# Kernel tuning notes

Measured on AMD Instinct MI355X. Metric: run time of the kernel, lower is better.

## Reference

```python
import jax, jax.numpy as jnp
import numpy as np

D_MODEL = 1024
NUM_HEADS = 16
HEAD_DIM = D_MODEL // NUM_HEADS


def setup_inputs() -> dict:
    key = jax.random.key(0)
    ks = jax.random.split(key, 10)
    B, SQ, SK = 2, 2048, 2048
    scale = 1.0 / np.sqrt(D_MODEL)
    inp = {
        "x1": jax.random.normal(ks[0], (B, SQ, D_MODEL), jnp.float32),
        "x2": jax.random.normal(ks[1], (B, SK, D_MODEL), jnp.float32),
        "Wq": jax.random.normal(ks[2], (D_MODEL, D_MODEL), jnp.float32) * scale,
        "bq": jnp.zeros((D_MODEL,), jnp.float32),
        "Wk": jax.random.normal(ks[3], (D_MODEL, D_MODEL), jnp.float32) * scale,
        "bk": jnp.zeros((D_MODEL,), jnp.float32),
        "Wv": jax.random.normal(ks[4], (D_MODEL, D_MODEL), jnp.float32) * scale,
        "bv": jnp.zeros((D_MODEL,), jnp.float32),
        "Wo": jax.random.normal(ks[5], (D_MODEL, D_MODEL), jnp.float32) * scale,
        "bo": jnp.zeros((D_MODEL,), jnp.float32),
    }
    return inp


def reference(x1, x2, Wq, bq, Wk, bk, Wv, bv, Wo, bo):
    B, SQ, _ = x1.shape
    SK = x2.shape[1]
    # projections, then split into heads: [B, H, S, Dh]
    def split_heads(t, S):
        return t.reshape(B, S, NUM_HEADS, HEAD_DIM).transpose(0, 2, 1, 3)
    Q = split_heads(x1 @ Wq + bq, SQ)
    K = split_heads(x2 @ Wk + bk, SK)
    V = split_heads(x2 @ Wv + bv, SK)
    # note: original scales by 1/head_dim**0.5
    scores = jnp.einsum("bhqd,bhkd->bhqk", Q, K) / jnp.sqrt(
        jnp.asarray(HEAD_DIM, Q.dtype))
    attn = jax.nn.softmax(scores, axis=-1)
    ctx = jnp.einsum("bhqk,bhkd->bhqd", attn, V)
    ctx = ctx.transpose(0, 2, 1, 3).reshape(B, SQ, D_MODEL)
    return ctx @ Wo + bo
```

## Files before the change

kernel.cpp:

```cpp
#include <hip/hip_runtime.h>
#include <stdint.h>


typedef unsigned short u16b;
typedef __attribute__((ext_vector_type(4))) short short4v;
typedef __attribute__((ext_vector_type(8))) short short8v;
typedef __attribute__((ext_vector_type(4))) float float4v;
typedef __attribute__((ext_vector_type(2))) unsigned int uint2v;

#if __has_builtin(__builtin_amdgcn_exp2f)
__device__ __forceinline__ float exp2_fast(float x){ return __builtin_amdgcn_exp2f(x); }
#else
__device__ __forceinline__ float exp2_fast(float x){ return exp2f(x); }
#endif

__device__ __forceinline__ float bf2f(u16b u) {
  union { unsigned int i; float f; } v; v.i = ((unsigned int)u) << 16; return v.f;
}
__device__ __forceinline__ u16b f2bf(float f) {
  union { float f; unsigned int i; } v; v.f = f;
  return (u16b)((v.i + 0x7fffu + ((v.i >> 16) & 1u)) >> 16);
}
__device__ __forceinline__ void gl_lds16(const u16b* g, u16b* l) {
  __builtin_amdgcn_global_load_lds(
      (const __attribute__((address_space(1))) void*)g,
      (__attribute__((address_space(3))) void*)l, 16, 0, 0);
}

__global__ __launch_bounds__(256) void cvt2_bf16(
    const float* __restrict__ s0, const float* __restrict__ s1,
    u16b* __restrict__ d0, u16b* __restrict__ d1, int n4) {
  const float* src = blockIdx.y ? s1 : s0;
  u16b* dst = blockIdx.y ? d1 : d0;
  int i = blockIdx.x * blockDim.x + threadIdx.x;
  int stride = gridDim.x * blockDim.x;
  for (; i < n4; i += stride) {
    float4v v = ((const float4v*)src)[i];
    short4v o;
    o[0]=(short)f2bf(v[0]); o[1]=(short)f2bf(v[1]);
    o[2]=(short)f2bf(v[2]); o[3]=(short)f2bf(v[3]);
    ((short4v*)dst)[i] = o;
  }
}

__global__ __launch_bounds__(256) void transposeW(
    const float* __restrict__ W0, const float* __restrict__ W1,
    const float* __restrict__ W2, const float* __restrict__ W3,
    u16b* __restrict__ out) {
  __shared__ u16b tile[32][33];
  const int z = blockIdx.z;
  const float* src = (z==0) ? W0 : (z==1) ? W1 : (z==2) ? W2 : W3;
  u16b* dst = out + (size_t)z * (1024*1024);
  const int x = threadIdx.x, y = threadIdx.y;
  const int bx = blockIdx.x * 32, by = blockIdx.y * 32;
#pragma unroll
  for (int j=0;j<4;++j)
    tile[y*4+j][x] = f2bf(src[(size_t)(by + y*4+j)*1024 + bx + x]);
  __syncthreads();
#pragma unroll
  for (int j=0;j<4;++j)
    dst[(size_t)(bx + y*4+j)*1024 + by + x] = tile[x][y*4+j];
}

template<int BN, bool OUT_F32>
__device__ __forceinline__ void gemm_core(
    const u16b* __restrict__ A, const u16b* __restrict__ Bt,
    const float* __restrict__ bias, void* __restrict__ Cv,
    int N, int K, int bm, int bn) {
  constexpr int NT = BN / 32;
  __shared__ __align__(16) u16b As[128*32];
  __shared__ __align__(16) u16b Bs[BN*32];
  const int tid = threadIdx.x;
  const int lane = tid & 63, wave = tid >> 6;
  const int wm = wave >> 1, wn = wave & 1;
  const int l15 = lane & 15, l4 = lane >> 4;
  float4v acc[4][NT];
#pragma unroll
  for (int i=0;i<4;++i)
#pragma unroll
    for (int j=0;j<NT;++j) acc[i][j] = (float4v){0.f,0.f,0.f,0.f};

  const int swz = (l15 >> 1) & 3;

  for (int k0 = 0; k0 < K; k0 += 32) {
    __syncthreads();
    {
      int row = tid >> 2, seg = tid & 3;
      int segg0 = seg ^ ((row >> 1) & 3);
      int row2 = row + 64;
      int segg1 = seg ^ ((row2 >> 1) & 3);
      gl_lds16(&A[(size_t)(bm+row )*K + k0 + segg0*8], &As[tid*8]);
      gl_lds16(&A[(size_t)(bm+row2)*K + k0 + segg1*8], &As[(tid+256)*8]);
      gl_lds16(&Bt[(size_t)(bn+row )*K + k0 + segg0*8], &Bs[tid*8]);
      if (BN == 128)
        gl_lds16(&Bt[(size_t)(bn+row2)*K + k0 + segg1*8], &Bs[(tid+256)*8]);
    }
    __syncthreads();
    short8v af[4], bf[NT];
#pragma unroll
    for (int mt=0;mt<4;++mt)
      af[mt] = *(const short8v*)&As[(wm*64+mt*16+l15)*32 + ((l4 ^ swz)*8)];
#pragma unroll
    for (int nt=0;nt<NT;++nt)
      bf[nt] = *(const short8v*)&Bs[(wn*(BN/2)+nt*16+l15)*32 + ((l4 ^ swz)*8)];
#pragma unroll
    for (int mt=0;mt<4;++mt)
#pragma unroll
      for (int nt=0;nt<NT;++nt)
        acc[mt][nt] = __builtin_amdgcn_mfma_f32_16x16x32_bf16(af[mt], bf[nt], acc[mt][nt], 0, 0, 0);
  }

#pragma unroll
  for (int nt=0;nt<NT;++nt) {
    int col = bn + wn*(BN/2) + nt*16 + l15;
    float bb = bias[col];
#pragma unroll
    for (int mt=0;mt<4;++mt) {
      int row0 = bm + wm*64 + mt*16 + l4*4;
#pragma unroll
      for (int r=0;r<4;++r) {
        float v = acc[mt][nt][r] + bb;
        if (OUT_F32) ((float*)Cv)[(size_t)(row0+r)*N + col] = v;
        else         ((u16b*)Cv)[(size_t)(row0+r)*N + col] = f2bf(v);
      }
    }
  }
}

__global__ __launch_bounds__(256) void gemm_qkv(
    const u16b* __restrict__ x1b, const u16b* __restrict__ x2b,
    const u16b* __restrict__ WT, const float* __restrict__ bq,
    const float* __restrict__ bk, const float* __restrict__ bv,
    u16b* __restrict__ out) {
  const int z = blockIdx.z;
  const u16b* A = (z == 0) ? x1b : x2b;
  const u16b* Bt = WT + (size_t)z * (1024*1024);
  const float* bias = (z == 0) ? bq : (z == 1) ? bk : bv;
  u16b* C = out + (size_t)z * (4u*1024*1024);
  gemm_core<128,false>(A, Bt, bias, C, 1024, 1024, blockIdx.y*128, blockIdx.x*128);
}

__global__ __launch_bounds__(256) void gemm_out(
    const u16b* __restrict__ A, const u16b* __restrict__ Bt,
    const float* __restrict__ bias, float* __restrict__ C) {
  gemm_core<64,true>(A, Bt, bias, C, 1024, 1024, blockIdx.y*128, blockIdx.x*64);
}

__global__ __launch_bounds__(256) void attn128(
    const u16b* __restrict__ Q, const u16b* __restrict__ Kg,
    const u16b* __restrict__ Vg, u16b* __restrict__ O) {
  __shared__ __align__(16) u16b Ks[64*64];
  __shared__ __align__(16) u16b Vs[64*72];
  __shared__ __align__(16) u16b Ps[4*2*16*72];
  const int tid = threadIdx.x;
  const int lane = tid & 63, wave = tid >> 6;
  const int l15 = lane & 15, l4 = lane >> 4;
  const int h = blockIdx.y, b = blockIdx.z;
  const int q0 = blockIdx.x * 128;
  const size_t seqbase = (size_t)b * 2048;
  const int colh = h * 64;
  u16b* Pw = Ps + wave * 2304;

  const float qscale = 0.125f * 1.4426950408889634f;
  short8v qf[2][2];
#pragma unroll
  for (int g=0; g<2; ++g) {
    size_t qrow = seqbase + q0 + wave*32 + g*16 + l15;
#pragma unroll
    for (int ks=0; ks<2; ++ks) {
      short8v raw = *(const short8v*)&Q[qrow*1024 + colh + ks*32 + l4*8];
      short8v s;
#pragma unroll
      for (int i=0;i<8;++i) s[i] = (short)f2bf(bf2f((u16b)raw[i]) * qscale);
      qf[g][ks] = s;
    }
  }

  float lpart[2] = {0.f, 0.f};
  float4v oacc[2][4];
#pragma unroll
  for (int g=0; g<2; ++g)
#pragma unroll
    for (int nb=0; nb<4; ++nb) oacc[g][nb] = (float4v){0.f,0.f,0.f,0.f};

  const int vseg = tid >> 5;
  const int vrp  = tid & 31;

  for (int kt = 0; kt < 32; ++kt) {
    const size_t kvbase = seqbase + (size_t)kt*64;
    __syncthreads();
#pragma unroll
    for (int j=0; j<2; ++j) {
      int idx = j*256 + tid;
      int row = idx >> 3, seg = idx & 7;
      int segg = seg ^ (row & 7);
      gl_lds16(&Kg[(kvbase+row)*1024 + colh + segg*8], &Ks[idx*8]);
    }
    {
      short8v v0 = *(const short8v*)&Vg[(kvbase + 2*vrp    )*1024 + colh + vseg*8];
      short8v v1 = *(const short8v*)&Vg[(kvbase + 2*vrp + 1)*1024 + colh + vseg*8];
#pragma unroll
      for (int i=0;i<8;++i) {
        unsigned int val = (unsigned int)(u16b)v0[i] | ((unsigned int)(u16b)v1[i] << 16);
        *(unsigned int*)&Vs[(vseg*8+i)*72 + 2*vrp] = val;
      }
    }
    __syncthreads();

    float4v sacc[2][4];
#pragma unroll
    for (int g=0; g<2; ++g)
#pragma unroll
      for (int nb=0; nb<4; ++nb) sacc[g][nb] = (float4v){0.f,0.f,0.f,0.f};
#pragma unroll
    for (int nb=0; nb<4; ++nb)
#pragma unroll
      for (int ks=0; ks<2; ++ks) {
        short8v kf = *(const short8v*)&Ks[(nb*16+l15)*64 + (((ks*4+l4) ^ (l15 & 7))*8)];
        sacc[0][nb] = __builtin_amdgcn_mfma_f32_16x16x32_bf16(kf, qf[0][ks], sacc[0][nb], 0, 0, 0);
        sacc[1][nb] = __builtin_amdgcn_mfma_f32_16x16x32_bf16(kf, qf[1][ks], sacc[1][nb], 0, 0, 0);
      }

#pragma unroll
    for (int g=0; g<2; ++g) {
      float ls = 0.f;
#pragma unroll
      for (int nb=0; nb<4; ++nb) {
        unsigned int u0, u1, u2, u3;
        u0 = __float_as_uint(exp2_fast(sacc[g][nb][0]));
        u1 = __float_as_uint(exp2_fast(sacc[g][nb][1]));
        u2 = __float_as_uint(exp2_fast(sacc[g][nb][2]));
        u3 = __float_as_uint(exp2_fast(sacc[g][nb][3]));
        ls += __uint_as_float(u0 & 0xFFFF0000u) + __uint_as_float(u1 & 0xFFFF0000u)
            + __uint_as_float(u2 & 0xFFFF0000u) + __uint_as_float(u3 & 0xFFFF0000u);
        uint2v dw;
        dw[0] = (u0 >> 16) | (u1 & 0xFFFF0000u);
        dw[1] = (u2 >> 16) | (u3 & 0xFFFF0000u);
        *(uint2v*)&Pw[g*1152 + l15*72 + nb*16 + l4*4] = dw;
      }
      lpart[g] += ls;
    }

    __asm__ __volatile__("s_waitcnt lgkmcnt(0)" ::: "memory");

#pragma unroll
    for (int ks=0; ks<2; ++ks) {
      short8v pf0 = *(const short8v*)&Pw[       l15*72 + ks*32 + l4*8];
      short8v pf1 = *(const short8v*)&Pw[1152 + l15*72 + ks*32 + l4*8];
#pragma unroll
      for (int nb=0; nb<4; ++nb) {
        short8v vf = *(const short8v*)&Vs[(nb*16+l15)*72 + ks*32 + l4*8];
        oacc[0][nb] = __builtin_amdgcn_mfma_f32_16x16x32_bf16(pf0, vf, oacc[0][nb], 0, 0, 0);
        oacc[1][nb] = __builtin_amdgcn_mfma_f32_16x16x32_bf16(pf1, vf, oacc[1][nb], 0, 0, 0);
      }
    }
  }

#pragma unroll
  for (int g=0; g<2; ++g) {
    float l = lpart[g];
    l += __shfl_xor(l, 16);
    l += __shfl_xor(l, 32);
#pragma unroll
    for (int r=0; r<4; ++r) {
      float ld = __shfl(l, (lane & 48) | (l4*4 + r), 64);
      float inv = 1.0f / ld;
      size_t row = seqbase + q0 + wave*32 + g*16 + l4*4 + r;
#pragma unroll
      for (int nb=0; nb<4; ++nb)
        O[row*1024 + colh + nb*16 + l15] = f2bf(oacc[g][nb][r] * inv);
    }
  }
}

extern "C" void kernel_launch(void* const* d_in, const int* in_sizes, int n_in,
                              void* d_out, int out_size, void* d_ws, size_t ws_size,
                              hipStream_t stream) {
  const float* x1 = (const float*)d_in[0];
  const float* x2 = (const float*)d_in[1];
  const float* Wq = (const float*)d_in[2];
  const float* bq = (const float*)d_in[3];
  const float* Wk = (const float*)d_in[4];
  const float* bk = (const float*)d_in[5];
  const float* Wv = (const float*)d_in[6];
  const float* bv = (const float*)d_in[7];
  const float* Wo = (const float*)d_in[8];
  const float* bo = (const float*)d_in[9];
  (void)in_sizes; (void)n_in; (void)out_size; (void)ws_size;

  u16b* ws = (u16b*)d_ws;
  const size_t Mi = 1024*1024;
  u16b* WT  = ws;
  u16b* WoT = ws + 3*Mi;
  u16b* x1b = ws + 4*Mi;
  u16b* x2b = ws + 8*Mi;
  u16b* QKV = ws + 12*Mi;
  u16b* Qb  = QKV;
  u16b* Kb  = QKV + 4*Mi;
  u16b* Vb  = QKV + 8*Mi;
  u16b* Cx  = x1b;

  cvt2_bf16<<<dim3(1024,2), 256, 0, stream>>>(x1, x2, x1b, x2b, (int)Mi);
  transposeW<<<dim3(32,32,4), dim3(32,8,1), 0, stream>>>(Wq, Wk, Wv, Wo, WT);

  gemm_qkv<<<dim3(8,32,3), 256, 0, stream>>>(x1b, x2b, WT, bq, bk, bv, QKV);

  attn128<<<dim3(16,16,2), 256, 0, stream>>>(Qb, Kb, Vb, Cx);

  gemm_out<<<dim3(16,32), 256, 0, stream>>>(Cx, WoT, bo, (float*)d_out);
}
```

Measured before the change: 226.7 us.

## Write V transposed from QKV GEMM and double attention KV tile to 128

New measurement: 231.0 us. No clear change (+1.9%).

```diff
diff --git a/kernel.cpp b/kernel.cpp
--- a/kernel.cpp
+++ b/kernel.cpp
@@ -62,7 +62,7 @@
     dst[(size_t)(bx + y*4+j)*1024 + by + x] = tile[x][y*4+j];
 }
 
-template<int BN, bool OUT_F32>
+template<int BN, int OM>
 __device__ __forceinline__ void gemm_core(
     const u16b* __restrict__ A, const u16b* __restrict__ Bt,
     const float* __restrict__ bias, void* __restrict__ Cv,
@@ -117,11 +117,19 @@
 #pragma unroll
     for (int mt=0;mt<4;++mt) {
       int row0 = bm + wm*64 + mt*16 + l4*4;
-#pragma unroll
-      for (int r=0;r<4;++r) {
-        float v = acc[mt][nt][r] + bb;
-        if (OUT_F32) ((float*)Cv)[(size_t)(row0+r)*N + col] = v;
-        else         ((u16b*)Cv)[(size_t)(row0+r)*N + col] = f2bf(v);
+      if (OM == 2) {
+        int bloc = row0 >> 11, kv0 = row0 & 2047;
+        uint2v dw;
+        dw[0] = (unsigned)f2bf(acc[mt][nt][0] + bb) | ((unsigned)f2bf(acc[mt][nt][1] + bb) << 16);
+        dw[1] = (unsigned)f2bf(acc[mt][nt][2] + bb) | ((unsigned)f2bf(acc[mt][nt][3] + bb) << 16);
+        *(uint2v*)((u16b*)Cv + ((size_t)(bloc*1024 + col))*2048 + kv0) = dw;
+      } else {
+#pragma unroll
+        for (int r=0;r<4;++r) {
+          float v = acc[mt][nt][r] + bb;
+          if (OM == 1) ((float*)Cv)[(size_t)(row0+r)*N + col] = v;
+          else         ((u16b*)Cv)[(size_t)(row0+r)*N + col] = f2bf(v);
+        }
       }
     }
   }
@@ -135,22 +143,24 @@
   const int z = blockIdx.z;
   const u16b* A = (z == 0) ? x1b : x2b;
   const u16b* Bt = WT + (size_t)z * (1024*1024);
-  const float* bias = (z == 0) ? bq : (z == 1) ? bk : bv;
   u16b* C = out + (size_t)z * (4u*1024*1024);
-  gemm_core<128,false>(A, Bt, bias, C, 1024, 1024, blockIdx.y*128, blockIdx.x*128);
+  if (z == 2)
+    gemm_core<128,2>(A, Bt, bv, C, 1024, 1024, blockIdx.y*128, blockIdx.x*128);
+  else
+    gemm_core<128,0>(A, Bt, (z==0)?bq:bk, C, 1024, 1024, blockIdx.y*128, blockIdx.x*128);
 }
 
 __global__ __launch_bounds__(256) void gemm_out(
     const u16b* __restrict__ A, const u16b* __restrict__ Bt,
     const float* __restrict__ bias, float* __restrict__ C) {
-  gemm_core<64,true>(A, Bt, bias, C, 1024, 1024, blockIdx.y*128, blockIdx.x*64);
+  gemm_core<64,1>(A, Bt, bias, C, 1024, 1024, blockIdx.y*128, blockIdx.x*64);
 }
 
 __global__ __launch_bounds__(256) void attn128(
     const u16b* __restrict__ Q, const u16b* __restrict__ Kg,
-    const u16b* __restrict__ Vg, u16b* __restrict__ O) {
-  __shared__ __align__(16) u16b Ks[64*64];
-  __shared__ __align__(16) u16b Vs[64*72];
+    const u16b* __restrict__ Vt, u16b* __restrict__ O) {
+  __shared__ __align__(16) u16b Ks[128*64];
+  __shared__ __align__(16) u16b Vs[64*128];
   __shared__ __align__(16) u16b Ps[4*2*16*72];
   const int tid = threadIdx.x;
   const int lane = tid & 63, wave = tid >> 6;
@@ -159,6 +169,7 @@
   const int q0 = blockIdx.x * 128;
   const size_t seqbase = (size_t)b * 2048;
   const int colh = h * 64;
+  const int vtbase = (b*16 + h) * 64;
   u16b* Pw = Ps + wave * 2304;
 
   const float qscale = 0.125f * 1.4426950408889634f;
@@ -183,37 +194,31 @@
 #pragma unroll
     for (int nb=0; nb<4; ++nb) oacc[g][nb] = (float4v){0.f,0.f,0.f,0.f};
 
-  const int vseg = tid >> 5;
-  const int vrp  = tid & 31;
-
-  for (int kt = 0; kt < 32; ++kt) {
-    const size_t kvbase = seqbase + (size_t)kt*64;
+  for (int kt = 0; kt < 16; ++kt) {
+    const size_t kvbase = seqbase + (size_t)kt*128;
     __syncthreads();
 #pragma unroll
-    for (int j=0; j<2; ++j) {
+    for (int j=0; j<4; ++j) {
       int idx = j*256 + tid;
-      int row = idx >> 3, seg = idx & 7;
-      int segg = seg ^ (row & 7);
-      gl_lds16(&Kg[(kvbase+row)*1024 + colh + segg*8], &Ks[idx*8]);
-    }
-    {
-      short8v v0 = *(const short8v*)&Vg[(kvbase + 2*vrp    )*1024 + colh + vseg*8];
-      short8v v1 = *(const short8v*)&Vg[(kvbase + 2*vrp + 1)*1024 + colh + vseg*8];
-#pragma unroll
-      for (int i=0;i<8;++i) {
-        unsigned int val = (unsigned int)(u16b)v0[i] | ((unsigned int)(u16b)v1[i] << 16);
-        *(unsigned int*)&Vs[(vseg*8+i)*72 + 2*vrp] = val;
+      {
+        int row = idx >> 3, seg = idx & 7;
+        gl_lds16(&Kg[(kvbase+row)*1024 + colh + ((seg ^ (row & 7))*8)], &Ks[idx*8]);
+      }
+      {
+        int row = idx >> 4, seg = idx & 15;
+        gl_lds16(&Vt[(size_t)(vtbase+row)*2048 + (size_t)kt*128 + ((seg ^ (row & 15))*8)],
+                 &Vs[idx*8]);
       }
     }
     __syncthreads();
 
-    float4v sacc[2][4];
+    float4v sacc[2][8];
 #pragma unroll
     for (int g=0; g<2; ++g)
 #pragma unroll
-      for (int nb=0; nb<4; ++nb) sacc[g][nb] = (float4v){0.f,0.f,0.f,0.f};
-#pragma unroll
-    for (int nb=0; nb<4; ++nb)
+      for (int nb=0; nb<8; ++nb) sacc[g][nb] = (float4v){0.f,0.f,0.f,0.f};
+#pragma unroll
+    for (int nb=0; nb<8; ++nb)
 #pragma unroll
       for (int ks=0; ks<2; ++ks) {
         short8v kf = *(const short8v*)&Ks[(nb*16+l15)*64 + (((ks*4+l4) ^ (l15 & 7))*8)];
@@ -222,36 +227,39 @@
       }
 
 #pragma unroll
-    for (int g=0; g<2; ++g) {
-      float ls = 0.f;
-#pragma unroll
-      for (int nb=0; nb<4; ++nb) {
-        unsigned int u0, u1, u2, u3;
-        u0 = __float_as_uint(exp2_fast(sacc[g][nb][0]));
-        u1 = __float_as_uint(exp2_fast(sacc[g][nb][1]));
-        u2 = __float_as_uint(exp2_fast(sacc[g][nb][2]));
-        u3 = __float_as_uint(exp2_fast(sacc[g][nb][3]));
-        ls += __uint_as_float(u0 & 0xFFFF0000u) + __uint_as_float(u1 & 0xFFFF0000u)
-            + __uint_as_float(u2 & 0xFFFF0000u) + __uint_as_float(u3 & 0xFFFF0000u);
-        uint2v dw;
-        dw[0] = (u0 >> 16) | (u1 & 0xFFFF0000u);
-        dw[1] = (u2 >> 16) | (u3 & 0xFFFF0000u);
-        *(uint2v*)&Pw[g*1152 + l15*72 + nb*16 + l4*4] = dw;
-      }
-      lpart[g] += ls;
-    }
-
-    __asm__ __volatile__("s_waitcnt lgkmcnt(0)" ::: "memory");
-
-#pragma unroll
-    for (int ks=0; ks<2; ++ks) {
-      short8v pf0 = *(const short8v*)&Pw[       l15*72 + ks*32 + l4*8];
-      short8v pf1 = *(const short8v*)&Pw[1152 + l15*72 + ks*32 + l4*8];
-#pragma unroll
-      for (int nb=0; nb<4; ++nb) {
-        short8v vf = *(const short8v*)&Vs[(nb*16+l15)*72 + ks*32 + l4*8];
-        oacc[0][nb] = __builtin_amdgcn_mfma_f32_16x16x32_bf16(pf0, vf, oacc[0][nb], 0, 0, 0);
-        oacc[1][nb] = __builtin_amdgcn_mfma_f32_16x16x32_bf16(pf1, vf, oacc[1][nb], 0, 0, 0);
+    for (int h2=0; h2<2; ++h2) {
+#pragma unroll
+      for (int g=0; g<2; ++g) {
+        float ls = 0.f;
+#pragma unroll
+        for (int nbl=0; nbl<4; ++nbl) {
+          const float4v s4 = sacc[g][h2*4 + nbl];
+          unsigned int u0 = __float_as_uint(exp2_fast(s4[0]));
+          unsigned int u1 = __float_as_uint(exp2_fast(s4[1]));
+          unsigned int u2 = __float_as_uint(exp2_fast(s4[2]));
+          unsigned int u3 = __float_as_uint(exp2_fast(s4[3]));
+          ls += __uint_as_float(u0 & 0xFFFF0000u) + __uint_as_float(u1 & 0xFFFF0000u)
+              + __uint_as_float(u2 & 0xFFFF0000u) + __uint_as_float(u3 & 0xFFFF0000u);
+          uint2v dw;
+          dw[0] = (u0 >> 16) | (u1 & 0xFFFF0000u);
+          dw[1] = (u2 >> 16) | (u3 & 0xFFFF0000u);
+          *(uint2v*)&Pw[g*1152 + l15*72 + nbl*16 + l4*4] = dw;
+        }
+        lpart[g] += ls;
+      }
+      __asm__ __volatile__("s_waitcnt lgkmcnt(0)" ::: "memory");
+
+#pragma unroll
+      for (int ks2=0; ks2<2; ++ks2) {
+        short8v pf0 = *(const short8v*)&Pw[       l15*72 + ks2*32 + l4*8];
+        short8v pf1 = *(const short8v*)&Pw[1152 + l15*72 + ks2*32 + l4*8];
+#pragma unroll
+        for (int nb=0; nb<4; ++nb) {
+          int cc = (h2*8 + ks2*4 + l4) ^ l15;
+          short8v vf = *(const short8v*)&Vs[(nb*16+l15)*128 + cc*8];
+          oacc[0][nb] = __builtin_amdgcn_mfma_f32_16x16x32_bf16(pf0, vf, oacc[0][nb], 0, 0, 0);
+          oacc[1][nb] = __builtin_amdgcn_mfma_f32_16x16x32_bf16(pf1, vf, oacc[1][nb], 0, 0, 0);
+        }
       }
     }
   }
@@ -297,7 +305,7 @@
   u16b* QKV = ws + 12*Mi;
   u16b* Qb  = QKV;
   u16b* Kb  = QKV + 4*Mi;
-  u16b* Vb  = QKV + 8*Mi;
+  u16b* Vtb = QKV + 8*Mi;
   u16b* Cx  = x1b;
 
   cvt2_bf16<<<dim3(1024,2), 256, 0, stream>>>(x1, x2, x1b, x2b, (int)Mi);
@@ -305,7 +313,7 @@
 
   gemm_qkv<<<dim3(8,32,3), 256, 0, stream>>>(x1b, x2b, WT, bq, bk, bv, QKV);
 
-  attn128<<<dim3(16,16,2), 256, 0, stream>>>(Qb, Kb, Vb, Cx);
+  attn128<<<dim3(16,16,2), 256, 0, stream>>>(Qb, Kb, Vtb, Cx);
 
   gemm_out<<<dim3(16,32), 256, 0, stream>>>(Cx, WoT, bo, (float*)d_out);
 }
```
